# Kernel tuning notes

Hardware: AMD Instinct MI355X
Metric: run time of the kernel (lower is better)

## Reference

```python
import jax, jax.numpy as jnp
import numpy as np

B, T, C = 2, 2048, 2048
N_HEAD, N_GROUPS, HEAD_SIZE = 32, 8, 64
Q_PER_KV = N_HEAD // N_GROUPS
ROPE_N_ELEM = HEAD_SIZE  # rotary_percentage = 1.0
ROPE_BASE = 10000


def build_rope_cache(seq_len, n_elem, base=ROPE_BASE):
    theta = 1.0 / (base ** (jnp.arange(0, n_elem, 2, dtype=jnp.float32) / n_elem))
    idx_theta = jnp.outer(jnp.arange(seq_len, dtype=jnp.float32), theta)  # (T, n_elem/2)
    idx_theta = jnp.concatenate([idx_theta, idx_theta], axis=-1)  # (T, n_elem)
    return jnp.cos(idx_theta), jnp.sin(idx_theta)


def apply_rope(x, cos, sin):
    # x: (..., T, n_elem); cos/sin: (T, n_elem)
    h = x.shape[-1]
    x1, x2 = x[..., : h // 2], x[..., h // 2 :]
    rotated = jnp.concatenate([-x2, x1], axis=-1)
    return x * cos + rotated * sin


def setup_inputs() -> dict:
    key = jax.random.key(0)
    ks = jax.random.split(key, 5)
    x = jax.random.normal(ks[0], (B, T, C), dtype=jnp.float32)
    attn_w = jax.random.normal(ks[1], ((N_HEAD + 2 * N_GROUPS) * HEAD_SIZE, C), dtype=jnp.float32) * 0.02
    attn_b = jax.random.normal(ks[2], ((N_HEAD + 2 * N_GROUPS) * HEAD_SIZE,), dtype=jnp.float32) * 0.02
    proj_w = jax.random.normal(ks[3], (C, N_HEAD * HEAD_SIZE), dtype=jnp.float32) * 0.02
    proj_b = jax.random.normal(ks[4], (C,), dtype=jnp.float32) * 0.02
    cos, sin = build_rope_cache(T, ROPE_N_ELEM)
    return {"x": x, "cos": cos, "sin": sin, "attn_w": attn_w, "attn_b": attn_b,
            "proj_w": proj_w, "proj_b": proj_b}


def reference(x, cos, sin, attn_w, attn_b, proj_w, proj_b):
    b, t, _ = x.shape
    # fused QKV projection
    qkv = x @ attn_w.T + attn_b  # (B, T, (nh + 2g)*hs)
    qkv = qkv.reshape(b, t, N_GROUPS, Q_PER_KV + 2, HEAD_SIZE)
    qkv = qkv.transpose(0, 2, 3, 1, 4)  # (B, G, q_per_kv+2, T, hs)
    q = qkv[:, :, :Q_PER_KV]            # (B, G, q_per_kv, T, hs)
    k = qkv[:, :, Q_PER_KV]             # (B, G, T, hs)
    v = qkv[:, :, Q_PER_KV + 1]         # (B, G, T, hs)
    # RoPE (rope_n_elem == head_size, so applies to the full head dim)
    q = apply_rope(q, cos, sin)
    k = apply_rope(k, cos, sin)
    # grouped-query causal SDPA (equivalent to expanding k/v across q_per_kv)
    scale = 1.0 / jnp.sqrt(jnp.float32(HEAD_SIZE))
    scores = jnp.einsum("bgqtd,bgsd->bgqts", q, k) * scale  # (B,G,qk,T,T)
    causal = jnp.tril(jnp.ones((t, t), dtype=bool))
    scores = jnp.where(causal, scores, -jnp.inf)
    att = jax.nn.softmax(scores, axis=-1)
    y = jnp.einsum("bgqts,bgsd->bgqtd", att, v)  # (B,G,qk,T,hs)
    # merge (G, q_per_kv) -> n_head, then (B, T, nh*hs)
    y = y.reshape(b, N_HEAD, t, HEAD_SIZE).transpose(0, 2, 1, 3).reshape(b, t, N_HEAD * HEAD_SIZE)
    return y @ proj_w.T + proj_b


if __name__ == "__main__":
    out = reference(**setup_inputs())
    print(out.shape, out.dtype)
```

## Files before the change

kernel.cpp:

```cpp
#include <hip/hip_runtime.h>

#define T_SEQ 2048
#define CDIM  2048
#define NH    32
#define NG    8
#define HS    64
#define NQKV  3072
#define MROWS 4096
#define BATCH 2

typedef __bf16          bf16x8  __attribute__((ext_vector_type(8)));
typedef float           f32x4   __attribute__((ext_vector_type(4)));
typedef unsigned short  ushortx8 __attribute__((ext_vector_type(8)));
typedef unsigned short  ushortx4 __attribute__((ext_vector_type(4)));

__device__ __forceinline__ unsigned short f2bf(float f) {
    unsigned int u = __float_as_uint(f);
    u += 0x7fffu + ((u >> 16) & 1u);
    return (unsigned short)(u >> 16);
}
__device__ __forceinline__ float bf2f(unsigned short h) {
    return __uint_as_float(((unsigned int)h) << 16);
}
__device__ __forceinline__ bf16x8 as_bf(ushortx8 u) {
    return __builtin_bit_cast(bf16x8, u);
}
__device__ __forceinline__ void gload16(const void* g, void* l) {
    __builtin_amdgcn_global_load_lds(
        (const __attribute__((address_space(1))) unsigned int*)g,
        (__attribute__((address_space(3))) unsigned int*)l, 16, 0, 0);
}

__global__ void f2bf_vec(const float* __restrict__ in, unsigned short* __restrict__ out, int n4) {
    int i = blockIdx.x * blockDim.x + threadIdx.x;
    if (i < n4) {
        float4 v = ((const float4*)in)[i];
        ushortx4 o;
        o[0] = f2bf(v.x); o[1] = f2bf(v.y); o[2] = f2bf(v.z); o[3] = f2bf(v.w);
        ((ushortx4*)out)[i] = o;
    }
}

template<int MODE>
__global__ __launch_bounds__(256)
void gemm_bt(const unsigned short* __restrict__ A, const float* __restrict__ Bt,
             const float* __restrict__ bias, int M, int N, int K,
             float* __restrict__ Cout,
             unsigned short* __restrict__ Qb, unsigned short* __restrict__ Kb,
             unsigned short* __restrict__ Vb) {
    const int tid  = threadIdx.x;
    const int lane = tid & 63, w = tid >> 6;
    const int grp  = lane >> 4, cc = lane & 15;
    const int wm   = w >> 1, wn = w & 1;
    const int m0   = blockIdx.y * 128, n0 = blockIdx.x * 128;

    __shared__ unsigned short Al[128 * 48];
    __shared__ unsigned short Bl[128 * 48];

    f32x4 acc[4][4];
#pragma unroll
    for (int i = 0; i < 4; i++)
#pragma unroll
        for (int j = 0; j < 4; j++) acc[i][j] = (f32x4)0.0f;

    const int r0 = tid >> 2;
    const int k8 = (tid & 3) * 8;

    for (int k0 = 0; k0 < K; k0 += 32) {
        ushortx8 av0 = *(const ushortx8*)(A + (long)(m0 + r0)      * K + k0 + k8);
        ushortx8 av1 = *(const ushortx8*)(A + (long)(m0 + 64 + r0) * K + k0 + k8);
        const float* bp0 = Bt + (long)(n0 + r0)      * K + k0 + k8;
        const float* bp1 = Bt + (long)(n0 + 64 + r0) * K + k0 + k8;
        float4 b0a = *(const float4*)bp0, b0b = *(const float4*)(bp0 + 4);
        float4 b1a = *(const float4*)bp1, b1b = *(const float4*)(bp1 + 4);
        ushortx8 bv0, bv1;
        bv0[0] = f2bf(b0a.x); bv0[1] = f2bf(b0a.y); bv0[2] = f2bf(b0a.z); bv0[3] = f2bf(b0a.w);
        bv0[4] = f2bf(b0b.x); bv0[5] = f2bf(b0b.y); bv0[6] = f2bf(b0b.z); bv0[7] = f2bf(b0b.w);
        bv1[0] = f2bf(b1a.x); bv1[1] = f2bf(b1a.y); bv1[2] = f2bf(b1a.z); bv1[3] = f2bf(b1a.w);
        bv1[4] = f2bf(b1b.x); bv1[5] = f2bf(b1b.y); bv1[6] = f2bf(b1b.z); bv1[7] = f2bf(b1b.w);
        __syncthreads();
        *(ushortx8*)(Al + r0 * 48 + k8)        = av0;
        *(ushortx8*)(Al + (64 + r0) * 48 + k8) = av1;
        *(ushortx8*)(Bl + r0 * 48 + k8)        = bv0;
        *(ushortx8*)(Bl + (64 + r0) * 48 + k8) = bv1;
        __syncthreads();

        bf16x8 af[4], bfr[4];
#pragma unroll
        for (int mi = 0; mi < 4; mi++)
            af[mi] = as_bf(*(ushortx8*)(Al + (wm * 64 + mi * 16 + cc) * 48 + grp * 8));
#pragma unroll
        for (int ni = 0; ni < 4; ni++)
            bfr[ni] = as_bf(*(ushortx8*)(Bl + (wn * 64 + ni * 16 + cc) * 48 + grp * 8));
#pragma unroll
        for (int mi = 0; mi < 4; mi++)
#pragma unroll
            for (int ni = 0; ni < 4; ni++)
                acc[mi][ni] = __builtin_amdgcn_mfma_f32_16x16x32_bf16(af[mi], bfr[ni], acc[mi][ni], 0, 0, 0);
    }

    if (MODE == 1) {
#pragma unroll
        for (int ni = 0; ni < 4; ni++) {
            const int col = n0 + wn * 64 + ni * 16 + cc;
            const float bb = bias[col];
#pragma unroll
            for (int mi = 0; mi < 4; mi++) {
                const int row = m0 + wm * 64 + mi * 16 + grp * 4;
#pragma unroll
                for (int j = 0; j < 4; j++)
                    Cout[(long)(row + j) * N + col] = acc[mi][ni][j] + bb;
            }
        }
    } else {
        const int slot = (n0 + wn * 64) >> 6;
        const int g = slot / 6, s = slot % 6;
        const int b = m0 >> 11;
        const int t0 = (m0 & (T_SEQ - 1)) + wm * 64;
        unsigned short* dst;
        if (s < 4)        dst = Qb + (long)((b * NH + g * 4 + s) * T_SEQ) * HS;
        else if (s == 4)  dst = Kb + (long)((b * NG + g) * T_SEQ) * HS;
        else              dst = Vb + (long)((b * NG + g) * T_SEQ) * HS;
#pragma unroll
        for (int ni = 0; ni < 4; ni++) {
            const int d = ni * 16 + cc;
            const float bb = bias[slot * 64 + d];
#pragma unroll
            for (int mi = 0; mi < 4; mi++) {
                const int t = t0 + mi * 16 + grp * 4;
#pragma unroll
                for (int j = 0; j < 4; j++)
                    dst[(long)(t + j) * HS + d] = f2bf(acc[mi][ni][j] + bb);
            }
        }
    }
}

__global__ void rope_kernel(unsigned short* __restrict__ Qb, unsigned short* __restrict__ Kb,
                            const float* __restrict__ cosT, const float* __restrict__ sinT) {
    const float QSC = 0.125f * 1.44269504088896340736f;
    long idx = (long)blockIdx.x * blockDim.x + threadIdx.x;
    const long NQP = (long)BATCH * NH * T_SEQ * 32;
    const long NKP = (long)BATCH * NG * T_SEQ * 32;
    unsigned short* base; float sc; long r; int dp;
    if (idx < NQP)            { base = Qb; sc = QSC;  r = idx >> 5;          dp = (int)(idx & 31); }
    else if (idx < NQP + NKP) { long k = idx - NQP; base = Kb; sc = 1.0f; r = k >> 5; dp = (int)(k & 31); }
    else return;
    const int t = (int)(r & (T_SEQ - 1));
    unsigned short* p = base + r * 64;
    float x1 = bf2f(p[dp]), x2 = bf2f(p[dp + 32]);
    float cv = cosT[t * 64 + dp], sv = sinT[t * 64 + dp];
    p[dp]      = f2bf((x1 * cv - x2 * sv) * sc);
    p[dp + 32] = f2bf((x2 * cv + x1 * sv) * sc);
}

__global__ __launch_bounds__(256, 3)
void attn_kernel(const unsigned short* __restrict__ Qb, const unsigned short* __restrict__ Kb,
                 const unsigned short* __restrict__ Vb, unsigned short* __restrict__ Yb) {
    const int dsp = blockIdx.x;
    const int wk  = (dsp & 7) * 64 + (dsp >> 3);
    const int bxp = wk & 7;
    const int h   = (wk >> 3) & 31;
    const int b   = wk >> 8;

    const int tid = threadIdx.x, lane = tid & 63, w = tid >> 6;
    const int grp = lane >> 4, cc = lane & 15;
    const int g = h >> 2;
    const unsigned short* Qh = Qb + (long)((b * NH + h) * T_SEQ) * HS;
    const unsigned short* Kh = Kb + (long)((b * NG + g) * T_SEQ) * HS;
    const unsigned short* Vh = Vb + (long)((b * NG + g) * T_SEQ) * HS;

    __shared__ unsigned short Kl[2][4096];
    __shared__ unsigned short Vt[2][80 * 72];
    __shared__ unsigned short Pl[4][32 * 72];

    for (int i = tid; i < 2 * 16 * 72; i += 256) {
        int buf = i / (16 * 72), rem = i % (16 * 72);
        int r = rem / 72, c = rem % 72;
        Vt[buf][(64 + r) * 72 + c] = (r == 0) ? (unsigned short)0x3F80 : (unsigned short)0;
    }

    const int U0 = (w * 2) * 64 + lane, U1 = U0 + 64;
    const int gk0 = (U0 >> 3) * 64 + (((U0 & 7) ^ ((U0 >> 3) & 7)) * 8);
    const int gk1 = (U1 >> 3) * 64 + (((U1 & 7) ^ ((U1 >> 3) & 7)) * 8);
    const int du0 = (w * 2) * 512, du1 = (w * 2 + 1) * 512;

    const int vp = tid & 31, vc = tid >> 5;
    const long vsrc = (long)(2 * vp) * HS + 8 * vc;

    for (int pass = 0; pass < 2; ++pass) {
        const int qtile = pass ? (15 - bxp) : bxp;
        const int q0  = qtile * 128;
        const int qrb = q0 + w * 32;
        const int NT  = 2 * qtile + 2;

        bf16x8 aq[2][2];
#pragma unroll
        for (int qh = 0; qh < 2; qh++)
#pragma unroll
            for (int kh = 0; kh < 2; kh++)
                aq[qh][kh] = as_bf(*(const ushortx8*)(Qh + (long)(qrb + qh * 16 + cc) * HS + kh * 32 + grp * 8));

        f32x4 o[2][5];
#pragma unroll
        for (int qh = 0; qh < 2; qh++)
#pragma unroll
            for (int dt = 0; dt < 5; dt++) o[qh][dt] = (f32x4)0.0f;
        float mr[2][4];
#pragma unroll
        for (int qh = 0; qh < 2; qh++)
#pragma unroll
            for (int j = 0; j < 4; j++) mr[qh][j] = -1e30f;

        {
            gload16(Kh + gk0, &Kl[0][du0]);
            gload16(Kh + gk1, &Kl[0][du1]);
            ushortx8 v0 = *(const ushortx8*)(Vh + vsrc);
            ushortx8 v1 = *(const ushortx8*)(Vh + vsrc + HS);
#pragma unroll
            for (int e = 0; e < 8; e++) {
                unsigned int pk = (unsigned int)v0[e] | ((unsigned int)v1[e] << 16);
                *(unsigned int*)&Vt[0][(8 * vc + e) * 72 + 2 * vp] = pk;
            }
        }
        __syncthreads();

        for (int t = 0; t < NT; ++t) {
            const int cur = t & 1;
            const bool pre = (t + 1 < NT);
            ushortx8 v0, v1;
            if (pre) {
                const long kofs = (long)(t + 1) * 64 * HS;
                v0 = *(const ushortx8*)(Vh + kofs + vsrc);
                v1 = *(const ushortx8*)(Vh + kofs + vsrc + HS);
                gload16(Kh + kofs + gk0, &Kl[cur ^ 1][du0]);
                gload16(Kh + kofs + gk1, &Kl[cur ^ 1][du1]);
            }
            const int kv0 = t * 64;
            if (kv0 <= qrb + 31) {
                bf16x8 kf[4][2];
#pragma unroll
                for (int ct = 0; ct < 4; ct++)
#pragma unroll
                    for (int kh = 0; kh < 2; kh++)
                        kf[ct][kh] = as_bf(*(const ushortx8*)&Kl[cur][(ct * 16 + cc) * 64 + (((kh * 4 + grp) ^ (cc & 7)) * 8)]);
                f32x4 s[2][4];
                __builtin_amdgcn_s_setprio(1);
#pragma unroll
                for (int qh = 0; qh < 2; qh++)
#pragma unroll
                    for (int ct = 0; ct < 4; ct++) {
                        f32x4 a = (f32x4)0.0f;
                        a = __builtin_amdgcn_mfma_f32_16x16x32_bf16(aq[qh][0], kf[ct][0], a, 0, 0, 0);
                        a = __builtin_amdgcn_mfma_f32_16x16x32_bf16(aq[qh][1], kf[ct][1], a, 0, 0, 0);
                        s[qh][ct] = a;
                    }
                __builtin_amdgcn_s_setprio(0);
                if (kv0 + 63 > qrb) {
#pragma unroll
                    for (int qh = 0; qh < 2; qh++)
#pragma unroll
                        for (int ct = 0; ct < 4; ct++)
#pragma unroll
                            for (int j = 0; j < 4; j++) {
                                int col = kv0 + ct * 16 + cc, row = qrb + qh * 16 + grp * 4 + j;
                                if (col > row) s[qh][ct][j] = -1e30f;
                            }
                }
#pragma unroll
                for (int qh = 0; qh < 2; qh++) {
                    float pm[4];
#pragma unroll
                    for (int j = 0; j < 4; j++) {
                        float v = fmaxf(fmaxf(s[qh][0][j], s[qh][1][j]), fmaxf(s[qh][2][j], s[qh][3][j]));
                        v = fmaxf(v, __shfl_xor(v, 1));
                        v = fmaxf(v, __shfl_xor(v, 2));
                        v = fmaxf(v, __shfl_xor(v, 4));
                        v = fmaxf(v, __shfl_xor(v, 8));
                        pm[j] = v;
                    }
                    bool need = false;
#pragma unroll
                    for (int j = 0; j < 4; j++) need |= (pm[j] > mr[qh][j] + 8.0f);
                    if (__any(need)) {
                        float al[4];
#pragma unroll
                        for (int j = 0; j < 4; j++) {
                            float mn = fmaxf(mr[qh][j], pm[j]);
                            al[j] = exp2f(mr[qh][j] - mn);
                            mr[qh][j] = mn;
                        }
#pragma unroll
                        for (int dt = 0; dt < 5; dt++)
#pragma unroll
                            for (int j = 0; j < 4; j++) o[qh][dt][j] *= al[j];
                    }
#pragma unroll
                    for (int ct = 0; ct < 4; ct++)
#pragma unroll
                        for (int j = 0; j < 4; j++)
                            s[qh][ct][j] = exp2f(s[qh][ct][j] - mr[qh][j]);
                }
#pragma unroll
                for (int qh = 0; qh < 2; qh++)
#pragma unroll
                    for (int ct = 0; ct < 4; ct++)
#pragma unroll
                        for (int j = 0; j < 4; j++)
                            Pl[w][(qh * 16 + grp * 4 + j) * 72 + ct * 16 + cc] = f2bf(s[qh][ct][j]);
                bf16x8 pa[2][2];
#pragma unroll
                for (int qh = 0; qh < 2; qh++)
#pragma unroll
                    for (int kc = 0; kc < 2; kc++)
                        pa[qh][kc] = as_bf(*(ushortx8*)&Pl[w][(qh * 16 + cc) * 72 + kc * 32 + grp * 8]);
                __builtin_amdgcn_s_setprio(1);
#pragma unroll
                for (int dt = 0; dt < 5; dt++) {
                    bf16x8 vb[2];
#pragma unroll
                    for (int kc = 0; kc < 2; kc++)
                        vb[kc] = as_bf(*(const ushortx8*)&Vt[cur][(dt * 16 + cc) * 72 + kc * 32 + grp * 8]);
#pragma unroll
                    for (int qh = 0; qh < 2; qh++)
#pragma unroll
                        for (int kc = 0; kc < 2; kc++)
                            o[qh][dt] = __builtin_amdgcn_mfma_f32_16x16x32_bf16(pa[qh][kc], vb[kc], o[qh][dt], 0, 0, 0);
                }
                __builtin_amdgcn_s_setprio(0);
            }
            if (pre) {
#pragma unroll
                for (int e = 0; e < 8; e++) {
                    unsigned int pk = (unsigned int)v0[e] | ((unsigned int)v1[e] << 16);
                    *(unsigned int*)&Vt[cur ^ 1][(8 * vc + e) * 72 + 2 * vp] = pk;
                }
            }
            __syncthreads();
        }

#pragma unroll
        for (int qh = 0; qh < 2; qh++) {
            float inv[4];
#pragma unroll
            for (int j = 0; j < 4; j++) {
                float lrv = __shfl(o[qh][4][j], (lane & 48));
                inv[j] = 1.0f / lrv;
            }
#pragma unroll
            for (int dt = 0; dt < 4; dt++)
#pragma unroll
                for (int j = 0; j < 4; j++) {
                    int row = qrb + qh * 16 + grp * 4 + j;
                    Yb[((long)(b * T_SEQ + row)) * CDIM + h * HS + dt * 16 + cc] = f2bf(o[qh][dt][j] * inv[j]);
                }
        }
    }
}

extern "C" void kernel_launch(void* const* d_in, const int* in_sizes, int n_in,
                              void* d_out, int out_size, void* d_ws, size_t ws_size,
                              hipStream_t stream) {
    const float* x      = (const float*)d_in[0];
    const float* cosT   = (const float*)d_in[1];
    const float* sinT   = (const float*)d_in[2];
    const float* attn_w = (const float*)d_in[3];
    const float* attn_b = (const float*)d_in[4];
    const float* proj_w = (const float*)d_in[5];
    const float* proj_b = (const float*)d_in[6];
    float* out = (float*)d_out;

    char* p = (char*)d_ws;
    unsigned short* XY = (unsigned short*)p; p += (size_t)MROWS * CDIM * 2;
    unsigned short* Qb = (unsigned short*)p; p += (size_t)BATCH * NH * T_SEQ * HS * 2;
    unsigned short* Kb = (unsigned short*)p; p += (size_t)BATCH * NG * T_SEQ * HS * 2;
    unsigned short* Vb = (unsigned short*)p; p += (size_t)BATCH * NG * T_SEQ * HS * 2;

    f2bf_vec<<<(MROWS * CDIM / 4 + 255) / 256, 256, 0, stream>>>(x, XY, MROWS * CDIM / 4);

    gemm_bt<0><<<dim3(NQKV / 128, MROWS / 128), 256, 0, stream>>>(
        XY, attn_w, attn_b, MROWS, NQKV, CDIM, nullptr, Qb, Kb, Vb);

    {
        long npairs = (long)BATCH * NH * T_SEQ * 32 + (long)BATCH * NG * T_SEQ * 32;
        rope_kernel<<<(int)((npairs + 255) / 256), 256, 0, stream>>>(Qb, Kb, cosT, sinT);
    }

    attn_kernel<<<dim3((T_SEQ / 128 / 2) * NH * BATCH), 256, 0, stream>>>(Qb, Kb, Vb, XY);

    gemm_bt<1><<<dim3(CDIM / 128, MROWS / 128), 256, 0, stream>>>(
        XY, proj_w, proj_b, MROWS, CDIM, CDIM, out, nullptr, nullptr, nullptr);
}
```

Before: 399.7 us.

## Pre-convert weights to bf16 and stream GEMM tiles via global_load_lds with XOR swizzle

Adds a per-call pass that converts both weight matrices to bf16 in workspace, when the workspace is large enough. The GEMMs then load A and B tiles straight into LDS with global_load_lds into a 32-wide XOR-swizzled layout instead of going through registers. This removes the per-tile fp32-to-bf16 conversion and halves the weight bytes read inside the GEMM K loop. In exchange it adds two extra conversion kernels and extra workspace traffic on every call.

```diff
diff --git a/kernel.cpp b/kernel.cpp
--- a/kernel.cpp
+++ b/kernel.cpp
@@ -41,9 +41,10 @@
     }
 }
 
-template<int MODE>
+template<int MODE, int BBF>
 __global__ __launch_bounds__(256)
-void gemm_bt(const unsigned short* __restrict__ A, const float* __restrict__ Bt,
+void gemm_bt(const unsigned short* __restrict__ A,
+             const unsigned short* __restrict__ Btb, const float* __restrict__ Btf,
              const float* __restrict__ bias, int M, int N, int K,
              float* __restrict__ Cout,
              unsigned short* __restrict__ Qb, unsigned short* __restrict__ Kb,
@@ -54,7 +55,7 @@
     const int wm   = w >> 1, wn = w & 1;
     const int m0   = blockIdx.y * 128, n0 = blockIdx.x * 128;
 
-    __shared__ unsigned short Al[128 * 48];
+    __shared__ unsigned short Al[128 * 32];
     __shared__ unsigned short Bl[128 * 48];
 
     f32x4 acc[4][4];
@@ -63,35 +64,59 @@
 #pragma unroll
         for (int j = 0; j < 4; j++) acc[i][j] = (f32x4)0.0f;
 
+    const int U0 = w * 128 + lane, U1 = U0 + 64;
+    const int ar0 = U0 >> 2, ac0 = ((U0 & 3) ^ (ar0 & 3)) * 8;
+    const int ar1 = U1 >> 2, ac1 = ((U1 & 3) ^ (ar1 & 3)) * 8;
+    const unsigned short* as0 = A + (long)(m0 + ar0) * K + ac0;
+    const unsigned short* as1 = A + (long)(m0 + ar1) * K + ac1;
+    unsigned short* ad0 = Al + w * 1024;
+    unsigned short* ad1 = Al + w * 1024 + 512;
+
+    const unsigned short* bsv0 = nullptr; const unsigned short* bsv1 = nullptr;
+    unsigned short* bd0 = nullptr; unsigned short* bd1 = nullptr;
+    if (BBF) {
+        bsv0 = Btb + (long)(n0 + ar0) * K + ac0;
+        bsv1 = Btb + (long)(n0 + ar1) * K + ac1;
+        bd0 = Bl + w * 1024; bd1 = Bl + w * 1024 + 512;
+    }
     const int r0 = tid >> 2;
     const int k8 = (tid & 3) * 8;
 
     for (int k0 = 0; k0 < K; k0 += 32) {
-        ushortx8 av0 = *(const ushortx8*)(A + (long)(m0 + r0)      * K + k0 + k8);
-        ushortx8 av1 = *(const ushortx8*)(A + (long)(m0 + 64 + r0) * K + k0 + k8);
-        const float* bp0 = Bt + (long)(n0 + r0)      * K + k0 + k8;
-        const float* bp1 = Bt + (long)(n0 + 64 + r0) * K + k0 + k8;
-        float4 b0a = *(const float4*)bp0, b0b = *(const float4*)(bp0 + 4);
-        float4 b1a = *(const float4*)bp1, b1b = *(const float4*)(bp1 + 4);
-        ushortx8 bv0, bv1;
-        bv0[0] = f2bf(b0a.x); bv0[1] = f2bf(b0a.y); bv0[2] = f2bf(b0a.z); bv0[3] = f2bf(b0a.w);
-        bv0[4] = f2bf(b0b.x); bv0[5] = f2bf(b0b.y); bv0[6] = f2bf(b0b.z); bv0[7] = f2bf(b0b.w);
-        bv1[0] = f2bf(b1a.x); bv1[1] = f2bf(b1a.y); bv1[2] = f2bf(b1a.z); bv1[3] = f2bf(b1a.w);
-        bv1[4] = f2bf(b1b.x); bv1[5] = f2bf(b1b.y); bv1[6] = f2bf(b1b.z); bv1[7] = f2bf(b1b.w);
-        __syncthreads();
-        *(ushortx8*)(Al + r0 * 48 + k8)        = av0;
-        *(ushortx8*)(Al + (64 + r0) * 48 + k8) = av1;
-        *(ushortx8*)(Bl + r0 * 48 + k8)        = bv0;
-        *(ushortx8*)(Bl + (64 + r0) * 48 + k8) = bv1;
-        __syncthreads();
+        if (BBF) {
+            __syncthreads();
+            gload16(as0 + k0, ad0); gload16(as1 + k0, ad1);
+            gload16(bsv0 + k0, bd0); gload16(bsv1 + k0, bd1);
+            __syncthreads();
+        } else {
+            const float* bp0 = Btf + (long)(n0 + r0)      * K + k0 + k8;
+            const float* bp1 = Btf + (long)(n0 + 64 + r0) * K + k0 + k8;
+            float4 b0a = *(const float4*)bp0, b0b = *(const float4*)(bp0 + 4);
+            float4 b1a = *(const float4*)bp1, b1b = *(const float4*)(bp1 + 4);
+            ushortx8 bv0, bv1;
+            bv0[0] = f2bf(b0a.x); bv0[1] = f2bf(b0a.y); bv0[2] = f2bf(b0a.z); bv0[3] = f2bf(b0a.w);
+            bv0[4] = f2bf(b0b.x); bv0[5] = f2bf(b0b.y); bv0[6] = f2bf(b0b.z); bv0[7] = f2bf(b0b.w);
+            bv1[0] = f2bf(b1a.x); bv1[1] = f2bf(b1a.y); bv1[2] = f2bf(b1a.z); bv1[3] = f2bf(b1a.w);
+            bv1[4] = f2bf(b1b.x); bv1[5] = f2bf(b1b.y); bv1[6] = f2bf(b1b.z); bv1[7] = f2bf(b1b.w);
+            __syncthreads();
+            *(ushortx8*)(Bl + r0 * 48 + k8)        = bv0;
+            *(ushortx8*)(Bl + (64 + r0) * 48 + k8) = bv1;
+            gload16(as0 + k0, ad0); gload16(as1 + k0, ad1);
+            __syncthreads();
+        }
 
         bf16x8 af[4], bfr[4];
 #pragma unroll
-        for (int mi = 0; mi < 4; mi++)
-            af[mi] = as_bf(*(ushortx8*)(Al + (wm * 64 + mi * 16 + cc) * 48 + grp * 8));
-#pragma unroll
-        for (int ni = 0; ni < 4; ni++)
-            bfr[ni] = as_bf(*(ushortx8*)(Bl + (wn * 64 + ni * 16 + cc) * 48 + grp * 8));
+        for (int mi = 0; mi < 4; mi++) {
+            const int row = wm * 64 + mi * 16 + cc;
+            af[mi] = as_bf(*(ushortx8*)(Al + row * 32 + ((grp ^ (cc & 3)) * 8)));
+        }
+#pragma unroll
+        for (int ni = 0; ni < 4; ni++) {
+            const int row = wn * 64 + ni * 16 + cc;
+            bfr[ni] = BBF ? as_bf(*(ushortx8*)(Bl + row * 32 + ((grp ^ (cc & 3)) * 8)))
+                          : as_bf(*(ushortx8*)(Bl + row * 48 + grp * 8));
+        }
 #pragma unroll
         for (int mi = 0; mi < 4; mi++)
 #pragma unroll
@@ -375,11 +400,23 @@
     unsigned short* Qb = (unsigned short*)p; p += (size_t)BATCH * NH * T_SEQ * HS * 2;
     unsigned short* Kb = (unsigned short*)p; p += (size_t)BATCH * NG * T_SEQ * HS * 2;
     unsigned short* Vb = (unsigned short*)p; p += (size_t)BATCH * NG * T_SEQ * HS * 2;
+    unsigned short* Wq = (unsigned short*)p; p += (size_t)NQKV * CDIM * 2;
+    unsigned short* Wp = (unsigned short*)p; p += (size_t)CDIM * CDIM * 2;
+    const size_t WS_NEED_BF = (size_t)(40 + 12 + 8) * 1024 * 1024;
+    const bool wbf = (ws_size >= WS_NEED_BF);
 
     f2bf_vec<<<(MROWS * CDIM / 4 + 255) / 256, 256, 0, stream>>>(x, XY, MROWS * CDIM / 4);
-
-    gemm_bt<0><<<dim3(NQKV / 128, MROWS / 128), 256, 0, stream>>>(
-        XY, attn_w, attn_b, MROWS, NQKV, CDIM, nullptr, Qb, Kb, Vb);
+    if (wbf) {
+        f2bf_vec<<<(NQKV * CDIM / 4 + 255) / 256, 256, 0, stream>>>(attn_w, Wq, NQKV * CDIM / 4);
+        f2bf_vec<<<(CDIM * CDIM / 4 + 255) / 256, 256, 0, stream>>>(proj_w, Wp, CDIM * CDIM / 4);
+    }
+
+    if (wbf)
+        gemm_bt<0, 1><<<dim3(NQKV / 128, MROWS / 128), 256, 0, stream>>>(
+            XY, Wq, nullptr, attn_b, MROWS, NQKV, CDIM, nullptr, Qb, Kb, Vb);
+    else
+        gemm_bt<0, 0><<<dim3(NQKV / 128, MROWS / 128), 256, 0, stream>>>(
+            XY, nullptr, attn_w, attn_b, MROWS, NQKV, CDIM, nullptr, Qb, Kb, Vb);
 
     {
         long npairs = (long)BATCH * NH * T_SEQ * 32 + (long)BATCH * NG * T_SEQ * 32;
@@ -388,6 +425,10 @@
 
     attn_kernel<<<dim3((T_SEQ / 128 / 2) * NH * BATCH), 256, 0, stream>>>(Qb, Kb, Vb, XY);
 
-    gemm_bt<1><<<dim3(CDIM / 128, MROWS / 128), 256, 0, stream>>>(
-        XY, proj_w, proj_b, MROWS, CDIM, CDIM, out, nullptr, nullptr, nullptr);
-}
+    if (wbf)
+        gemm_bt<1, 1><<<dim3(CDIM / 128, MROWS / 128), 256, 0, stream>>>(
+            XY, Wp, nullptr, proj_b, MROWS, CDIM, CDIM, out, nullptr, nullptr, nullptr);
+    else
+        gemm_bt<1, 0><<<dim3(CDIM / 128, MROWS / 128), 256, 0, stream>>>(
+            XY, nullptr, proj_w, proj_b, MROWS, CDIM, CDIM, out, nullptr, nullptr, nullptr);
+}
```

Measured after the change: 397.0 us. About the same (-0.7%).
